# Kernel optimization log

Measured on AMD Instinct MI355X. Metric: run time of the kernel, lower is better.

The kernel has to match this reference:

```python
import jax, jax.numpy as jnp
import numpy as np

IN_DIM = 9
HIDDEN = 32
SORT_K = 30


def setup_inputs() -> dict:
    key = jax.random.key(0)
    ks = jax.random.split(key, 16)
    N, E, G = 250000, 2500000, 2048
    x = jax.random.normal(ks[0], (N, IN_DIM), dtype=jnp.float32)
    edge_index = jax.random.randint(ks[1], (2, E), 0, N, dtype=jnp.int32)
    batch = jnp.sort(jax.random.randint(ks[2], (N,), 0, G, dtype=jnp.int32))
    s = lambda k, sh: jax.random.normal(k, sh, dtype=jnp.float32) * 0.05
    return {
        "x": x, "edge_index": edge_index, "batch": batch, "num_graphs": G,
        "W1": s(ks[3], (IN_DIM, HIDDEN)), "b1": jnp.zeros((HIDDEN,), jnp.float32),
        "W2": s(ks[4], (HIDDEN, HIDDEN)), "b2": jnp.zeros((HIDDEN,), jnp.float32),
        "W3": s(ks[5], (HIDDEN, HIDDEN)), "b3": jnp.zeros((HIDDEN,), jnp.float32),
        "cw1": s(ks[6], (16, HIDDEN, 5)), "cb1": jnp.zeros((16,), jnp.float32),
        "cw2": s(ks[7], (32, 16, 5)), "cb2": jnp.zeros((32,), jnp.float32),
        "lw1": s(ks[8], (32 * (SORT_K - 8), 128)), "lb1": jnp.zeros((128,), jnp.float32),
        "lw2": s(ks[9], (128, 1)), "lb2": jnp.zeros((1,), jnp.float32),
    }


def _gcn(x, W, b, src, dst, dis, n):
    # PyG-style GCNConv: sym-normalized A+I, linear transform first.
    h = x @ W                                     # [N, H]
    msg = h[src] * (dis[src] * dis[dst])[:, None]  # [E, H]
    agg = jax.ops.segment_sum(msg, dst, num_segments=n)
    agg = agg + h * (dis * dis)[:, None]           # self-loops
    return agg + b


def _sort_pool(x, batch, num_graphs, k):
    n, h = x.shape
    key = x[:, -1]
    order = jnp.lexsort((-key, batch))             # by graph, key descending
    xs = x[order]
    bs = batch[order]
    counts = jax.ops.segment_sum(jnp.ones((n,), jnp.int32), batch, num_segments=num_graphs)
    starts = jnp.cumsum(counts) - counts           # exclusive prefix sum
    pos = jnp.arange(n, dtype=jnp.int32) - starts[bs]
    valid = pos < k
    g = jnp.where(valid, bs, num_graphs)           # out-of-range -> dropped
    p = jnp.where(valid, pos, 0)
    out = jnp.zeros((num_graphs, k, h), x.dtype)
    return out.at[g, p].set(xs, mode="drop")


def _conv1d(x, w, b):
    # x: [B, C, T], w: [O, I, K]
    y = jax.lax.conv_general_dilated(x, w, window_strides=(1,), padding="VALID",
                                     dimension_numbers=("NCH", "OIH", "NCH"))
    return y + b[None, :, None]


def reference(x, edge_index, batch, num_graphs, W1, b1, W2, b2, W3, b3,
              cw1, cb1, cw2, cb2, lw1, lb1, lw2, lb2):
    n = x.shape[0]
    src, dst = edge_index[0], edge_index[1]
    deg = jax.ops.segment_sum(jnp.ones_like(src, dtype=x.dtype), dst, num_segments=n) + 1.0
    dis = jax.lax.rsqrt(deg)
    h = jax.nn.relu(_gcn(x, W1, b1, src, dst, dis, n))
    h = jax.nn.relu(_gcn(h, W2, b2, src, dst, dis, n))
    h = jax.nn.relu(_gcn(h, W3, b3, src, dst, dis, n))
    p = _sort_pool(h, batch, num_graphs, SORT_K)   # [G, K, H]
    p = jnp.transpose(p, (0, 2, 1))                # [G, H, K]
    p = jax.nn.relu(_conv1d(p, cw1, cb1))
    p = jax.nn.relu(_conv1d(p, cw2, cb2))
    p = p.reshape(num_graphs, -1)
    p = jax.nn.relu(p @ lw1 + lb1)
    return (p @ lw2 + lb2).reshape(-1)
```

## Files before the change

### kernel.cpp

```cpp
#include <hip/hip_runtime.h>

typedef unsigned long long ull;

#define HIDDEN 32
#define SORTK 30
#define KCAP 256
#define GPB 2
#define BSH 7
#define BNODES (1 << BSH)
#define BCAP 1536
#define HMAX 2048
#define NSEG 256
#define SRC_BITS 18
#define SRC_MASK ((1u << SRC_BITS) - 1)
#define EID_SH  SRC_BITS
#define LD_SH   (SRC_BITS + 22)

static inline int ceil_div_i(long long a, int b){ return (int)((a + b - 1) / b); }

__global__ __launch_bounds__(1024) void hist_kernel(const int* __restrict__ dsts,
                                                    int* __restrict__ hist,
                                                    int E, int NB, int segsz){
  __shared__ int h[HMAX];
  for (int i = threadIdx.x; i < NB; i += 1024) h[i] = 0;
  __syncthreads();
  int seg = blockIdx.x;
  int e0 = seg * segsz;
  int e1 = e0 + segsz; if (e1 > E) e1 = E;
  for (int e = e0 + threadIdx.x; e < e1; e += 1024)
    atomicAdd(&h[dsts[e] >> BSH], 1);
  __syncthreads();
  for (int i = threadIdx.x; i < NB; i += 1024) hist[seg * NB + i] = h[i];
}

__global__ __launch_bounds__(256) void segscanA(const int* __restrict__ hist,
                                                int* __restrict__ segoff,
                                                int* __restrict__ btot,
                                                int NB, int S){
  int wv = (blockIdx.x * 256 + threadIdx.x) >> 6;
  int lane = threadIdx.x & 63;
  if (wv >= NB) return;
  int b = wv;
  int run_base = 0;
  for (int chunk = 0; chunk < S; chunk += 64){
    int s = chunk + lane;
    int v = (s < S) ? hist[(size_t)s * NB + b] : 0;
    int x = v;
    #pragma unroll
    for (int o = 1; o < 64; o <<= 1){ int y = __shfl_up(x, o, 64); if (lane >= o) x += y; }
    if (s < S) segoff[(size_t)s * NB + b] = run_base + x - v;
    run_base += __shfl(x, 63, 64);
  }
  if (lane == 0) btot[b] = run_base;
}

__global__ __launch_bounds__(1024) void segscanB(const int* __restrict__ btot,
                                                 int* __restrict__ bbase, int NB){
  int t = threadIdx.x;
  int b0 = t * 2, b1 = t * 2 + 1;
  int v0 = (b0 < NB) ? btot[b0] : 0;
  int v1 = (b1 < NB) ? btot[b1] : 0;
  int pair = v0 + v1;
  int lane = t & 63, wid = t >> 6;
  int x = pair;
  for (int o = 1; o < 64; o <<= 1){ int y = __shfl_up(x, o, 64); if (lane >= o) x += y; }
  __shared__ int wsum[16]; __shared__ int woff[16];
  if (lane == 63) wsum[wid] = x;
  __syncthreads();
  if (t == 0){ int run = 0; for (int w = 0; w < 16; w++){ woff[w] = run; run += wsum[w]; } }
  __syncthreads();
  int excl = x - pair + woff[wid];
  if (b0 < NB) bbase[b0] = excl;
  if (b1 < NB) bbase[b1] = excl + v0;
}

__global__ __launch_bounds__(1024) void scatter_kernel(const int* __restrict__ dsts,
                                                       const int* __restrict__ srcs,
                                                       const int* __restrict__ segoff,
                                                       const int* __restrict__ bbase,
                                                       ull* __restrict__ staging,
                                                       int E, int NB, int segsz){
  __shared__ int cur[HMAX];
  int seg = blockIdx.x;
  for (int i = threadIdx.x; i < NB; i += 1024) cur[i] = segoff[seg * NB + i] + bbase[i];
  __syncthreads();
  int e0 = seg * segsz;
  int e1 = e0 + segsz; if (e1 > E) e1 = E;
  for (int e = e0 + threadIdx.x; e < e1; e += 1024){
    int d = dsts[e];
    int slot = atomicAdd(&cur[d >> BSH], 1);
    staging[slot] = ((ull)(d & (BNODES - 1)) << LD_SH) | ((ull)e << EID_SH)
                  | (ull)(unsigned)srcs[e];
  }
}

__global__ __launch_bounds__(BNODES) void bucket_sort_kernel(
    const int* __restrict__ bbase, const ull* __restrict__ staging,
    int* __restrict__ csr, int* __restrict__ offs,
    float* __restrict__ dis, int N, int NB, int E){
  __shared__ ull ebuf[BCAP];
  __shared__ ull obuf[BCAP];
  __shared__ int cnt[BNODES];
  __shared__ int cur[BNODES];
  __shared__ int base0[BNODES];
  __shared__ int w0tot;
  int b = blockIdx.x, t = threadIdx.x;
  int n0 = b << BSH;
  int n1 = n0 + BNODES; if (n1 > N) n1 = N;
  int gbeg = bbase[b];
  int gend = (b + 1 < NB) ? bbase[b + 1] : E;
  int cnt_all = gend - gbeg;
  cnt[t] = 0;
  __syncthreads();

  if (cnt_all <= BCAP){
    for (int i = t; i < cnt_all; i += BNODES){
      ull k = staging[gbeg + i];
      ebuf[i] = k;
      atomicAdd(&cnt[(int)(k >> LD_SH)], 1);
    }
    __syncthreads();
    int v = cnt[t];
    int lane = t & 63, wid = t >> 6;
    int x = v;
    for (int o = 1; o < 64; o <<= 1){ int y = __shfl_up(x, o, 64); if (lane >= o) x += y; }
    if (wid == 0 && lane == 63) w0tot = x;
    __syncthreads();
    int ls = x - v + (wid ? w0tot : 0);
    cur[t] = ls;
    base0[t] = ls;
    int n = n0 + t;
    if (n < n1){
      float dd = (float)v + 1.0f;
      dis[n]  = __fdiv_rn(1.0f, __fsqrt_rn(dd));
      offs[n] = gbeg + ls;
    }
    __syncthreads();
    for (int i = t; i < cnt_all; i += BNODES){
      ull k = ebuf[i];
      int pos = atomicAdd(&cur[(int)(k >> LD_SH)], 1);
      obuf[pos] = k;
    }
    __syncthreads();
    for (int i = t; i < cnt_all; i += BNODES){
      ull k = obuf[i];
      int nd = (int)(k >> LD_SH);
      int base = base0[nd];
      int vn = cnt[nd];
      int r = 0;
      for (int j = 0; j < vn; j++) r += (obuf[base + j] < k) ? 1 : 0;
      csr[gbeg + base + r] = (int)(k & SRC_MASK);
    }
  } else {
    int n = n0 + t;
    int deg = 0;
    if (n < n1){
      for (int i = gbeg; i < gend; i++) if ((int)(staging[i] >> LD_SH) == t) deg++;
      float dd = (float)deg + 1.0f;
      dis[n] = __fdiv_rn(1.0f, __fsqrt_rn(dd));
    }
    cnt[t] = (n < n1) ? deg : 0;
    __syncthreads();
    if (n < n1){
      int ls = gbeg; for (int q = 0; q < t; q++) ls += cnt[q];
      offs[n] = ls;
      ull prev = 0;
      for (int o = 0; o < deg; o++){
        ull best = ~0ull;
        for (int i = gbeg; i < gend; i++){
          ull k = staging[i];
          if ((int)(k >> LD_SH) == t && (o == 0 || k > prev) && k < best) best = k;
        }
        csr[ls + o] = (int)(best & SRC_MASK); prev = best;
      }
    }
  }
  if (b == 0 && t == 0) offs[N] = E;
}

template<int K>
__global__ void node_matmul(const float* __restrict__ xin, const float* __restrict__ W,
                            float* __restrict__ H, int N){
  __shared__ float Ws[K * 32];
  for (int i = threadIdx.x; i < K * 32; i += blockDim.x) Ws[i] = W[i];
  __syncthreads();
  int tid = blockIdx.x * blockDim.x + threadIdx.x;
  int n = tid >> 5, c = tid & 31;
  if (n >= N) return;
  const float* xr = xin + (size_t)n * K;
  float acc = 0.f;
  if constexpr ((K & 3) == 0){
    const float4* xr4 = (const float4*)xr;
    #pragma unroll
    for (int k4 = 0; k4 < K / 4; k4++){
      float4 xv = xr4[k4];
      acc = fmaf(xv.x, Ws[(k4 * 4 + 0) * 32 + c], acc);
      acc = fmaf(xv.y, Ws[(k4 * 4 + 1) * 32 + c], acc);
      acc = fmaf(xv.z, Ws[(k4 * 4 + 2) * 32 + c], acc);
      acc = fmaf(xv.w, Ws[(k4 * 4 + 3) * 32 + c], acc);
    }
  } else {
    #pragma unroll
    for (int k = 0; k < K; k++) acc = fmaf(xr[k], Ws[k * 32 + c], acc);
  }
  H[(size_t)n * 32 + c] = acc;
}

__device__ __forceinline__ float4 acc_edge(float4 a, float4 h, float w){
  a.x = __fadd_rn(a.x, __fmul_rn(h.x, w));
  a.y = __fadd_rn(a.y, __fmul_rn(h.y, w));
  a.z = __fadd_rn(a.z, __fmul_rn(h.z, w));
  a.w = __fadd_rn(a.w, __fmul_rn(h.w, w));
  return a;
}

__global__ __launch_bounds__(256) void agg_kernel(const float* __restrict__ H,
                           const int* __restrict__ offsets,
                           const int* __restrict__ csr, const float* __restrict__ dis,
                           const float* __restrict__ bias, float* __restrict__ A,
                           float* __restrict__ keyout, int N){
  int tid = blockIdx.x * 256 + threadIdx.x;
  int n = tid >> 3, qw = tid & 7;
  if (n >= N) return;
  const float4* __restrict__ H4 = (const float4*)H;
  float dn = dis[n];
  int s = offsets[n], e = offsets[n + 1];
  float4 acc = make_float4(0.f, 0.f, 0.f, 0.f);
  int i = s;
  for (; i + 8 <= e; i += 8){
    int s0 = csr[i],   s1 = csr[i+1], s2 = csr[i+2], s3 = csr[i+3];
    int s4 = csr[i+4], s5 = csr[i+5], s6 = csr[i+6], s7 = csr[i+7];
    float4 h0 = H4[(size_t)s0 * 8 + qw];
    float4 h1 = H4[(size_t)s1 * 8 + qw];
    float4 h2 = H4[(size_t)s2 * 8 + qw];
    float4 h3 = H4[(size_t)s3 * 8 + qw];
    float4 h4 = H4[(size_t)s4 * 8 + qw];
    float4 h5 = H4[(size_t)s5 * 8 + qw];
    float4 h6 = H4[(size_t)s6 * 8 + qw];
    float4 h7 = H4[(size_t)s7 * 8 + qw];
    float w0 = __fmul_rn(dis[s0], dn), w1 = __fmul_rn(dis[s1], dn);
    float w2 = __fmul_rn(dis[s2], dn), w3 = __fmul_rn(dis[s3], dn);
    float w4 = __fmul_rn(dis[s4], dn), w5 = __fmul_rn(dis[s5], dn);
    float w6 = __fmul_rn(dis[s6], dn), w7 = __fmul_rn(dis[s7], dn);
    acc = acc_edge(acc, h0, w0);
    acc = acc_edge(acc, h1, w1);
    acc = acc_edge(acc, h2, w2);
    acc = acc_edge(acc, h3, w3);
    acc = acc_edge(acc, h4, w4);
    acc = acc_edge(acc, h5, w5);
    acc = acc_edge(acc, h6, w6);
    acc = acc_edge(acc, h7, w7);
  }
  for (; i < e; i++){
    int sr = csr[i];
    float w = __fmul_rn(dis[sr], dn);
    acc = acc_edge(acc, H4[(size_t)sr * 8 + qw], w);
  }
  float4 hn = H4[(size_t)n * 8 + qw];
  float sw = __fmul_rn(dn, dn);
  float4 bb = ((const float4*)bias)[qw];
  float4 v;
  v.x = fmaxf(__fadd_rn(__fadd_rn(acc.x, __fmul_rn(hn.x, sw)), bb.x), 0.f);
  v.y = fmaxf(__fadd_rn(__fadd_rn(acc.y, __fmul_rn(hn.y, sw)), bb.y), 0.f);
  v.z = fmaxf(__fadd_rn(__fadd_rn(acc.z, __fmul_rn(hn.z, sw)), bb.z), 0.f);
  v.w = fmaxf(__fadd_rn(__fadd_rn(acc.w, __fmul_rn(hn.w, sw)), bb.w), 0.f);
  ((float4*)A)[(size_t)n * 8 + qw] = v;
  if (keyout != nullptr && qw == 7) keyout[n] = v.w;
}

__global__ void gstarts_kernel(const int* __restrict__ batch, int* __restrict__ gstarts,
                               int N, int G){
  int g = blockIdx.x * blockDim.x + threadIdx.x;
  if (g > G) return;
  int lo = 0, hi = N;
  while (lo < hi){ int mid = (lo + hi) >> 1; if (batch[mid] < g) lo = mid + 1; else hi = mid; }
  gstarts[g] = lo;
}

__global__ __launch_bounds__(512) void head_kernel(
    const float* __restrict__ A, const float* __restrict__ keys,
    const int* __restrict__ gstarts,
    const float* __restrict__ cw1, const float* __restrict__ cb1,
    const float* __restrict__ cw2, const float* __restrict__ cb2,
    const float* __restrict__ lw1, const float* __restrict__ lb1,
    const float* __restrict__ lw2, const float* __restrict__ lb2,
    float* __restrict__ out, int G){
  int t = threadIdx.x;
  int sub = t >> 8, lt = t & 255;
  int g = blockIdx.x * GPB + sub;

  __shared__ float w1s[16 * 32 * 5];
  __shared__ float w2s[32 * 16 * 5];
  __shared__ float bufA[GPB][960];
  __shared__ float bufB[GPB][416];
  __shared__ int   sel[GPB][SORTK];

  for (int i = t; i < 2560; i += 512) w1s[i] = cw1[i];
  for (int i = t; i < 2560; i += 512) w2s[i] = cw2[i];
  for (int i = lt; i < 960; i += 256) bufA[sub][i] = 0.f;

  bool valid = (g < G);
  int s = 0, c = 0;
  if (valid){ s = gstarts[g]; c = gstarts[g + 1] - s; }
  bool fast = valid && (c <= KCAP);
  if (fast)
    for (int i = lt; i < c; i += 256) bufB[sub][i] = keys[s + i];
  __syncthreads();

  if (valid){
    if (fast){
      for (int i = lt; i < c; i += 256){
        float ki = bufB[sub][i];
        int rank = 0;
        #pragma unroll 8
        for (int j = 0; j < c; j++){
          float kj = bufB[sub][j];
          rank += (kj > ki || (kj == ki && j < i)) ? 1 : 0;
        }
        if (rank < SORTK) sel[sub][rank] = i;
      }
    } else {
      for (int i = lt; i < c; i += 256){
        float ki = keys[s + i];
        int rank = 0;
        for (int j = 0; j < c; j++){
          float kj = keys[s + j];
          if (kj > ki || (kj == ki && j < i)){
            if (++rank >= SORTK) break;
          }
        }
        if (rank < SORTK) sel[sub][rank] = i;
      }
    }
  }
  __syncthreads();

  if (valid){
    int kk = c < SORTK ? c : SORTK;
    for (int q = lt; q < kk * 32; q += 256){
      int pos = q >> 5, ch = q & 31;
      bufA[sub][ch * 30 + pos] = A[(size_t)(s + sel[sub][pos]) * 32 + ch];
    }
  }
  __syncthreads();

  if (valid){
    for (int q = lt; q < 16 * 26; q += 256){
      int o = q / 26, tt = q - o * 26;
      float acc = cb1[o];
      const float* wo = &w1s[o * 160];
      #pragma unroll 4
      for (int i = 0; i < 32; i++){
        const float* si = &bufA[sub][i * 30 + tt];
        #pragma unroll
        for (int k = 0; k < 5; k++) acc = fmaf(si[k], wo[i * 5 + k], acc);
      }
      bufB[sub][q] = fmaxf(acc, 0.f);
    }
  }
  __syncthreads();

  if (valid){
    for (int q = lt; q < 32 * 22; q += 256){
      int o = q / 22, tt = q - o * 22;
      float acc = cb2[o];
      const float* wo = &w2s[o * 80];
      #pragma unroll 4
      for (int i = 0; i < 16; i++){
        const float* si = &bufB[sub][i * 26 + tt];
        #pragma unroll
        for (int k = 0; k < 5; k++) acc = fmaf(si[k], wo[i * 5 + k], acc);
      }
      bufA[sub][q] = fmaxf(acc, 0.f);
    }
  }
  __syncthreads();

  if (valid){
    int outi = lt & 127, half = lt >> 7;
    float acc = half ? 0.f : lb1[outi];
    const int j0 = half * 352;
    #pragma unroll 8
    for (int j = 0; j < 352; j++){
      int jj = j0 + j;
      acc = fmaf(bufA[sub][jj], lw1[(size_t)jj * 128 + outi], acc);
    }
    bufB[sub][half * 128 + outi] = acc;
  }
  __syncthreads();
  if (valid && lt < 128) bufB[sub][lt] = fmaxf(bufB[sub][lt] + bufB[sub][128 + lt], 0.f);
  __syncthreads();

  if (valid && lt < 64){
    float v = __fadd_rn(__fmul_rn(bufB[sub][lt], lw2[lt]),
                        __fmul_rn(bufB[sub][lt + 64], lw2[lt + 64]));
    #pragma unroll
    for (int o = 32; o > 0; o >>= 1) v += __shfl_xor(v, o, 64);
    if (lt == 0) out[g] = v + lb2[0];
  }
}

extern "C" void kernel_launch(void* const* d_in, const int* in_sizes, int n_in,
                              void* d_out, int out_size, void* d_ws, size_t ws_size,
                              hipStream_t stream){
  const float* x     = (const float*)d_in[0];
  const int*   ei    = (const int*)  d_in[1];
  const int*   batch = (const int*)  d_in[2];
  const float* W1  = (const float*)d_in[4];
  const float* b1  = (const float*)d_in[5];
  const float* W2  = (const float*)d_in[6];
  const float* b2  = (const float*)d_in[7];
  const float* W3  = (const float*)d_in[8];
  const float* b3  = (const float*)d_in[9];
  const float* cw1 = (const float*)d_in[10];
  const float* cb1 = (const float*)d_in[11];
  const float* cw2 = (const float*)d_in[12];
  const float* cb2 = (const float*)d_in[13];
  const float* lw1 = (const float*)d_in[14];
  const float* lb1 = (const float*)d_in[15];
  const float* lw2 = (const float*)d_in[16];
  const float* lb2 = (const float*)d_in[17];

  int N = in_sizes[0] / 9;
  int E = in_sizes[1] / 2;
  int G = out_size;
  const int* srcs = ei;
  const int* dsts = ei + E;
  int NB = ceil_div_i(N, BNODES);
  int segsz = ceil_div_i(E, NSEG);

  char* base = (char*)d_ws;
  size_t off = 0;
  auto alloc = [&](size_t bytes) -> void* {
    off = (off + 255) & ~(size_t)255;
    void* r = base + off; off += bytes; return r;
  };
  float* dis    = (float*)alloc((size_t)N * 4);
  float* H      = (float*)alloc((size_t)N * 32 * 4);
  float* A      = (float*)alloc((size_t)N * 32 * 4);
  float* keyarr = (float*)alloc((size_t)N * 4);
  int*   offs   = (int*)alloc((size_t)(N + 1) * 4);
  int*   csr    = (int*)alloc((size_t)E * 4);
  int*   gst    = (int*)alloc((size_t)(G + 1) * 4);
  int*   hist   = (int*)alloc((size_t)NSEG * NB * 4);
  int*   segoff = (int*)alloc((size_t)NSEG * NB * 4);
  int*   btot   = (int*)alloc((size_t)NB * 4);
  int*   bbase  = (int*)alloc((size_t)(NB + 1) * 4);
  ull*   staging = (ull*)H;
  (void)ws_size; (void)n_in;

  hist_kernel<<<NSEG, 1024, 0, stream>>>(dsts, hist, E, NB, segsz);
  segscanA<<<ceil_div_i(NB * 64, 256), 256, 0, stream>>>(hist, segoff, btot, NB, NSEG);
  segscanB<<<1, 1024, 0, stream>>>(btot, bbase, NB);
  scatter_kernel<<<NSEG, 1024, 0, stream>>>(dsts, srcs, segoff, bbase, staging, E, NB, segsz);
  bucket_sort_kernel<<<NB, BNODES, 0, stream>>>(bbase, staging, csr, offs, dis, N, NB, E);

  int ntm = ceil_div_i((long long)N * 32, 256);
  int nta = ceil_div_i((long long)N * 8, 256);
  node_matmul<9><<<ntm, 256, 0, stream>>>(x, W1, H, N);
  agg_kernel<<<nta, 256, 0, stream>>>(H, offs, csr, dis, b1, A, nullptr, N);
  node_matmul<32><<<ntm, 256, 0, stream>>>(A, W2, H, N);
  agg_kernel<<<nta, 256, 0, stream>>>(H, offs, csr, dis, b2, A, nullptr, N);
  node_matmul<32><<<ntm, 256, 0, stream>>>(A, W3, H, N);
  agg_kernel<<<nta, 256, 0, stream>>>(H, offs, csr, dis, b3, A, keyarr, N);

  gstarts_kernel<<<ceil_div_i(G + 1, 256), 256, 0, stream>>>(batch, gst, N, G);
  head_kernel<<<ceil_div_i(G, GPB), 512, 0, stream>>>(A, keyarr, gst, cw1, cb1, cw2, cb2,
                                                      lw1, lb1, lw2, lb2, (float*)d_out, G);
}
```

Before: 551.0 us.

## Fuse next-layer weight matmul into GCN aggregation kernel via lane shuffles

```diff
diff --git a/kernel.cpp b/kernel.cpp
--- a/kernel.cpp
+++ b/kernel.cpp
@@ -189,20 +189,8 @@
   if (n >= N) return;
   const float* xr = xin + (size_t)n * K;
   float acc = 0.f;
-  if constexpr ((K & 3) == 0){
-    const float4* xr4 = (const float4*)xr;
-    #pragma unroll
-    for (int k4 = 0; k4 < K / 4; k4++){
-      float4 xv = xr4[k4];
-      acc = fmaf(xv.x, Ws[(k4 * 4 + 0) * 32 + c], acc);
-      acc = fmaf(xv.y, Ws[(k4 * 4 + 1) * 32 + c], acc);
-      acc = fmaf(xv.z, Ws[(k4 * 4 + 2) * 32 + c], acc);
-      acc = fmaf(xv.w, Ws[(k4 * 4 + 3) * 32 + c], acc);
-    }
-  } else {
-    #pragma unroll
-    for (int k = 0; k < K; k++) acc = fmaf(xr[k], Ws[k * 32 + c], acc);
-  }
+  #pragma unroll
+  for (int k = 0; k < K; k++) acc = fmaf(xr[k], Ws[k * 32 + c], acc);
   H[(size_t)n * 32 + c] = acc;
 }
 
@@ -214,14 +202,12 @@
   return a;
 }
 
-__global__ __launch_bounds__(256) void agg_kernel(const float* __restrict__ H,
-                           const int* __restrict__ offsets,
-                           const int* __restrict__ csr, const float* __restrict__ dis,
-                           const float* __restrict__ bias, float* __restrict__ A,
-                           float* __restrict__ keyout, int N){
-  int tid = blockIdx.x * 256 + threadIdx.x;
-  int n = tid >> 3, qw = tid & 7;
-  if (n >= N) return;
+__device__ __forceinline__ float4 agg_body(const float* __restrict__ H,
+                                           const int* __restrict__ offsets,
+                                           const int* __restrict__ csr,
+                                           const float* __restrict__ dis,
+                                           const float* __restrict__ bias,
+                                           int n, int qw){
   const float4* __restrict__ H4 = (const float4*)H;
   float dn = dis[n];
   int s = offsets[n], e = offsets[n + 1];
@@ -264,8 +250,56 @@
   v.y = fmaxf(__fadd_rn(__fadd_rn(acc.y, __fmul_rn(hn.y, sw)), bb.y), 0.f);
   v.z = fmaxf(__fadd_rn(__fadd_rn(acc.z, __fmul_rn(hn.z, sw)), bb.z), 0.f);
   v.w = fmaxf(__fadd_rn(__fadd_rn(acc.w, __fmul_rn(hn.w, sw)), bb.w), 0.f);
+  return v;
+}
+
+__global__ __launch_bounds__(256) void agg_kernel(const float* __restrict__ H,
+                           const int* __restrict__ offsets,
+                           const int* __restrict__ csr, const float* __restrict__ dis,
+                           const float* __restrict__ bias, float* __restrict__ A,
+                           float* __restrict__ keyout, int N){
+  int tid = blockIdx.x * 256 + threadIdx.x;
+  int n = tid >> 3, qw = tid & 7;
+  if (n >= N) return;
+  float4 v = agg_body(H, offsets, csr, dis, bias, n, qw);
   ((float4*)A)[(size_t)n * 8 + qw] = v;
   if (keyout != nullptr && qw == 7) keyout[n] = v.w;
+}
+
+__global__ __launch_bounds__(256) void agg_mm_kernel(const float* __restrict__ H,
+                           const int* __restrict__ offsets,
+                           const int* __restrict__ csr, const float* __restrict__ dis,
+                           const float* __restrict__ bias,
+                           const float* __restrict__ Wn,
+                           float* __restrict__ H2, int N){
+  int tid = blockIdx.x * 256 + threadIdx.x;
+  int n = tid >> 3, qw = tid & 7;
+  if (n >= N) return;
+  float4 v = agg_body(H, offsets, csr, dis, bias, n, qw);
+
+  const float4* __restrict__ Wn4 = (const float4*)Wn;
+  float4 o = make_float4(0.f, 0.f, 0.f, 0.f);
+  #pragma unroll
+  for (int p = 0; p < 8; p++){
+    float4 hp;
+    hp.x = __shfl(v.x, p, 8);
+    hp.y = __shfl(v.y, p, 8);
+    hp.z = __shfl(v.z, p, 8);
+    hp.w = __shfl(v.w, p, 8);
+    float4 wa = Wn4[(4 * p + 0) * 8 + qw];
+    float4 wb = Wn4[(4 * p + 1) * 8 + qw];
+    float4 wc = Wn4[(4 * p + 2) * 8 + qw];
+    float4 wd = Wn4[(4 * p + 3) * 8 + qw];
+    o.x = fmaf(hp.x, wa.x, o.x); o.y = fmaf(hp.x, wa.y, o.y);
+    o.z = fmaf(hp.x, wa.z, o.z); o.w = fmaf(hp.x, wa.w, o.w);
+    o.x = fmaf(hp.y, wb.x, o.x); o.y = fmaf(hp.y, wb.y, o.y);
+    o.z = fmaf(hp.y, wb.z, o.z); o.w = fmaf(hp.y, wb.w, o.w);
+    o.x = fmaf(hp.z, wc.x, o.x); o.y = fmaf(hp.z, wc.y, o.y);
+    o.z = fmaf(hp.z, wc.z, o.z); o.w = fmaf(hp.z, wc.w, o.w);
+    o.x = fmaf(hp.w, wd.x, o.x); o.y = fmaf(hp.w, wd.y, o.y);
+    o.z = fmaf(hp.w, wd.z, o.z); o.w = fmaf(hp.w, wd.w, o.w);
+  }
+  ((float4*)H2)[(size_t)n * 8 + qw] = o;
 }
 
 __global__ void gstarts_kernel(const int* __restrict__ batch, int* __restrict__ gstarts,
@@ -458,10 +492,8 @@
   int ntm = ceil_div_i((long long)N * 32, 256);
   int nta = ceil_div_i((long long)N * 8, 256);
   node_matmul<9><<<ntm, 256, 0, stream>>>(x, W1, H, N);
-  agg_kernel<<<nta, 256, 0, stream>>>(H, offs, csr, dis, b1, A, nullptr, N);
-  node_matmul<32><<<ntm, 256, 0, stream>>>(A, W2, H, N);
-  agg_kernel<<<nta, 256, 0, stream>>>(H, offs, csr, dis, b2, A, nullptr, N);
-  node_matmul<32><<<ntm, 256, 0, stream>>>(A, W3, H, N);
+  agg_mm_kernel<<<nta, 256, 0, stream>>>(H, offs, csr, dis, b1, W2, A, N);
+  agg_mm_kernel<<<nta, 256, 0, stream>>>(A, offs, csr, dis, b2, W3, H, N);
   agg_kernel<<<nta, 256, 0, stream>>>(H, offs, csr, dis, b3, A, keyarr, N);
 
   gstarts_kernel<<<ceil_div_i(G + 1, 256), 256, 0, stream>>>(batch, gst, N, G);
```

New measurement: 478.2 us. 1.15x faster.
